# Performance work log

Hardware: AMD Instinct MI355X
Metric: run time of the kernel (lower is better)

## Reference

```python
import jax, jax.numpy as jnp
import numpy as np

D_MODEL = 2048
D_COMPARE = 2048
D_MEMORY = 2048
N_HEADS = 16
KV_HEADS = 4
KV_REPEAT = N_HEADS // KV_HEADS          # 4
C_HD = D_COMPARE // N_HEADS              # 128 compare head dim
M_HD = D_MEMORY // N_HEADS               # 128 memory head dim
TOTAL_OUT = D_COMPARE + KV_HEADS * C_HD + KV_HEADS * M_HD  # 3072


def setup_inputs() -> dict:
    key = jax.random.key(0)
    ks = jax.random.split(key, 5)
    b, t = 2, 2048
    x = jax.random.normal(ks[0], (b, t, D_MODEL), dtype=jnp.float32)
    s_in = 1.0 / np.sqrt(D_MODEL)
    s_out = 1.0 / np.sqrt(D_MEMORY)
    in_w = jax.random.uniform(ks[1], (TOTAL_OUT, D_MODEL), jnp.float32, -s_in, s_in)
    in_b = jax.random.uniform(ks[2], (TOTAL_OUT,), jnp.float32, -s_in, s_in)
    out_w = jax.random.uniform(ks[3], (D_MODEL, D_MEMORY), jnp.float32, -s_out, s_out)
    out_b = jax.random.uniform(ks[4], (D_MODEL,), jnp.float32, -s_out, s_out)
    return {"x": x, "in_w": in_w, "in_b": in_b, "out_w": out_w, "out_b": out_b}


def reference(x, in_w, in_b, out_w, out_b):
    b, t, _ = x.shape
    packed = jnp.einsum("btd,od->bto", x, in_w) + in_b          # [b,t,TOTAL_OUT]
    q, k, v = jnp.split(packed, [D_COMPARE, D_COMPARE + KV_HEADS * C_HD], axis=-1)
    # q: [b, kv, rep, t, hd] -- head h maps to kv group h // KV_REPEAT
    # (torch repeat_interleave on KV head dim == grouped reshape of q heads)
    q = q.reshape(b, t, KV_HEADS, KV_REPEAT, C_HD).transpose(0, 2, 3, 1, 4)
    k = k.reshape(b, t, KV_HEADS, C_HD).transpose(0, 2, 1, 3)   # [b,kv,t,hd]
    v = v.reshape(b, t, KV_HEADS, M_HD).transpose(0, 2, 1, 3)   # [b,kv,t,mhd]
    scale = 1.0 / np.sqrt(C_HD)
    scores = jnp.einsum("bgrqd,bgkd->bgrqk", q, k) * scale      # [b,kv,rep,t,t]
    attn = jax.nn.softmax(scores, axis=-1)
    y = jnp.einsum("bgrqk,bgkd->bgrqd", attn, v)                # [b,kv,rep,t,mhd]
    y = y.transpose(0, 3, 1, 2, 4).reshape(b, t, D_MEMORY)      # heads back in order
    return jnp.einsum("btm,dm->btd", y, out_w) + out_b
```

## Files before the change

kernel.cpp:

```cpp
#include <hip/hip_runtime.h>
#include <hip/hip_bf16.h>
#include <stdint.h>

#define DEV __device__ __forceinline__

typedef __attribute__((ext_vector_type(8))) short bf16x8;
typedef __attribute__((ext_vector_type(4))) float f32x4;
typedef __attribute__((ext_vector_type(16))) float f32x16;
typedef __attribute__((ext_vector_type(4))) unsigned u32x4;

DEV unsigned short f2bf(float f) {
  unsigned u = __builtin_bit_cast(unsigned, f);
  unsigned r = u + 0x7FFF + ((u >> 16) & 1);
  return (unsigned short)(r >> 16);
}

DEV unsigned short f2bfh(float f) {
  __bf16 h = (__bf16)f;
  return __builtin_bit_cast(unsigned short, h);
}

DEV unsigned cvtpk(float lo, float hi) {
  unsigned r;
  asm("v_cvt_pk_bf16_f32 %0, %1, %2" : "=v"(r) : "v"(lo), "v"(hi));
  return r;
}

DEV void plswap(unsigned &a, unsigned &b) {
  asm("v_permlane32_swap_b32 %0, %1" : "+v"(a), "+v"(b));
}

typedef __attribute__((address_space(1))) void gvoid;
typedef __attribute__((address_space(3))) void lvoid;

DEV void g2l16(const void* g, void* l) {
  __builtin_amdgcn_global_load_lds((gvoid*)g, (lvoid*)l, 16, 0, 0);
}

#define MFMA16(a, b, c) __builtin_amdgcn_mfma_f32_16x16x32_bf16(a, b, c, 0, 0, 0)
#define MFMA32(a, b, c) __builtin_amdgcn_mfma_f32_32x32x16_bf16(a, b, c, 0, 0, 0)

__global__ void k_cvt3(const float* __restrict__ x, unsigned short* __restrict__ xo, int nx4,
                       const float* __restrict__ w, unsigned short* __restrict__ wo, int nw4,
                       const float* __restrict__ v, unsigned short* __restrict__ vo, int nv4) {
  int i = blockIdx.x * blockDim.x + threadIdx.x;
  int stride = gridDim.x * blockDim.x;
  int tot = nx4 + nw4 + nv4;
  for (; i < tot; i += stride) {
    const float* src; unsigned short* dst; int j = i;
    if (j < nx4) { src = x; dst = xo; }
    else if ((j -= nx4) < nw4) { src = w; dst = wo; }
    else { j -= nw4; src = v; dst = vo; }
    float4 val = reinterpret_cast<const float4*>(src)[j];
    ushort4 o;
    o.x = f2bf(val.x); o.y = f2bf(val.y); o.z = f2bf(val.z); o.w = f2bf(val.w);
    reinterpret_cast<ushort4*>(dst)[j] = o;
  }
}

template<bool BF16OUT>
__global__ __launch_bounds__(256, 2) void k_gemm(
    const unsigned short* __restrict__ A, const unsigned short* __restrict__ B,
    const float* __restrict__ bias, void* __restrict__ C,
    int M, int N, int K) {
  __shared__ unsigned short As[128 * 32];
  __shared__ unsigned short Bs[128 * 32];
  int tid = threadIdx.x;
  int lane = tid & 63, wid = tid >> 6;
  int bm = blockIdx.y * 128, bn = blockIdx.x * 128;
  int wm = (wid >> 1) * 64, wn = (wid & 1) * 64;
  int row16 = lane & 15, kq = lane >> 4;
  f32x4 acc[4][4] = {};
  int r = tid >> 2, c = (tid & 3) * 8;
  const unsigned short* Ag = A + (size_t)(bm + r) * K + c;
  const unsigned short* Bg = B + (size_t)(bn + r) * K + c;
  for (int k0 = 0; k0 < K; k0 += 32) {
    g2l16(Ag + k0, &As[tid * 8]);
    g2l16(Ag + (size_t)64 * K + k0, &As[2048 + tid * 8]);
    g2l16(Bg + k0, &Bs[tid * 8]);
    g2l16(Bg + (size_t)64 * K + k0, &Bs[2048 + tid * 8]);
    __syncthreads();
    bf16x8 a[4], b[4];
#pragma unroll
    for (int m = 0; m < 4; m++) a[m] = *(const bf16x8*)&As[(wm + m * 16 + row16) * 32 + kq * 8];
#pragma unroll
    for (int n = 0; n < 4; n++) b[n] = *(const bf16x8*)&Bs[(wn + n * 16 + row16) * 32 + kq * 8];
    __builtin_amdgcn_s_setprio(1);
#pragma unroll
    for (int m = 0; m < 4; m++)
#pragma unroll
      for (int n = 0; n < 4; n++)
        acc[m][n] = MFMA16(a[m], b[n], acc[m][n]);
    __builtin_amdgcn_s_setprio(0);
    __syncthreads();
  }
#pragma unroll
  for (int n = 0; n < 4; n++) {
    int col = bn + wn + n * 16 + row16;
    float bv = bias[col];
#pragma unroll
    for (int m = 0; m < 4; m++) {
      int rw = bm + wm + m * 16 + kq * 4;
#pragma unroll
      for (int j = 0; j < 4; j++) {
        float v = acc[m][n][j] + bv;
        if (BF16OUT) ((unsigned short*)C)[(size_t)(rw + j) * N + col] = f2bf(v);
        else         ((float*)C)[(size_t)(rw + j) * N + col] = v;
      }
    }
  }
}

__global__ void k_pack(const unsigned short* __restrict__ packed, unsigned short* __restrict__ attp) {
  __shared__ unsigned short tile[64][136];
  int t = blockIdx.x, g = blockIdx.y;
  int b = g >> 2, kv = g & 3;
  int tid = threadIdx.x;
#pragma unroll
  for (int i = 0; i < 4; i++) {
    int tl = i * 16 + (tid >> 4);
    int d0 = (tid & 15) * 8;
    *(bf16x8*)&tile[tl][d0] =
        *(const bf16x8*)&packed[(size_t)(b * 2048 + t * 64 + tl) * 3072 + 2560 + kv * 128 + d0];
  }
  size_t obase = (size_t)(g * 32 + t) * 32 * 64 * 8;
#pragma unroll
  for (int f = 0; f < 4; f++) {
    int idx = f * 256 + tid;
    int frag = idx >> 6, lane = idx & 63;
    int l31 = lane & 31, h2 = lane >> 5;
    int kb2 = frag >> 3, kc = frag & 7;
    const unsigned short* src = &packed[(size_t)(b * 2048 + t * 64 + kb2 * 32 + l31) * 3072
                                        + 2048 + kv * 128 + (2 * kc + h2) * 8];
    *(bf16x8*)&attp[obase + (size_t)(frag * 64 + lane) * 8] = *(const bf16x8*)src;
  }
  __syncthreads();
#pragma unroll
  for (int f = 0; f < 4; f++) {
    int idx = f * 256 + tid;
    int f16 = idx >> 6, lane = idx & 63;
    int l31 = lane & 31, h2 = lane >> 5;
    int db = f16 >> 2, ks = f16 & 3;
    int d = 32 * db + l31;
    bf16x8 ov;
#pragma unroll
    for (int e = 0; e < 8; e++) ov[e] = (short)tile[(2 * ks + h2) * 8 + e][d];
    *(bf16x8*)&attp[obase + (size_t)((16 + f16) * 64 + lane) * 8] = ov;
  }
}

__global__ __launch_bounds__(256, 2) void k_flash(
    const unsigned short* __restrict__ packed,
    const unsigned short* __restrict__ attp,
    unsigned short* __restrict__ Y) {
  __shared__ unsigned short Qs[128 * 128];
  int tid = threadIdx.x, lane = tid & 63, wid = tid >> 6;
  int l31 = lane & 31, hi = lane >> 5;
  int kx = l31 & 15;
  int g = blockIdx.x;
  int s8 = g & 7;
  int b = s8 >> 2, kv = s8 & 3;
  int w = g >> 3;
  int h = kv * 4 + (w & 3);
  int qt = w >> 2;
  size_t prow = (size_t)b * 2048;

  {
    int rr = tid >> 4;
    int cc = ((tid & 15) ^ rr) * 8;
    const unsigned short* qg = packed + (prow + qt * 128 + rr) * 3072 + h * 128 + cc;
#pragma unroll
    for (int i = 0; i < 8; i++)
      g2l16(qg + (size_t)i * 16 * 3072, &Qs[i * 2048 + tid * 8]);
  }
  asm volatile("s_waitcnt vmcnt(0)" ::: "memory");
  __builtin_amdgcn_s_barrier();
  bf16x8 q[8];
  int qrow = wid * 32 + l31;
#pragma unroll
  for (int kc = 0; kc < 8; kc++)
    q[kc] = *(const bf16x8*)&Qs[qrow * 128 + (((2 * kc + hi) ^ kx) * 8)];
  asm volatile("s_waitcnt lgkmcnt(0)" ::: "memory");
  __builtin_amdgcn_sched_barrier(0);
  __builtin_amdgcn_s_barrier();

  const bf16x8* pk = (const bf16x8*)attp + ((size_t)s8 << 16);

  bf16x8 b0[4], b1[4], b2[4], b3[4];
#pragma unroll
  for (int j = 0; j < 4; j++) {
    b0[j] = pk[((0 + j) << 6) | lane];
    b1[j] = pk[((4 + j) << 6) | lane];
    b2[j] = pk[((8 + j) << 6) | lane];
    b3[j] = pk[((12 + j) << 6) | lane];
  }

  f32x16 o[4] = {};
  f32x16 ls = {};
  const float sc2 = 0.08838834764831845f * 1.4426950408889634f;
  const float MOFF = 14.f;
  bf16x8 ones;
#pragma unroll
  for (int e = 0; e < 8; e++) ones[e] = (short)0x3F80;

  for (int t = 0; t < 32; t++) {
    const bf16x8* pt  = pk + ((size_t)t << 11);
    const bf16x8* ptn = pk + ((size_t)(t < 31 ? t + 1 : 31) << 11);

    f32x16 st0 = {}, st1 = {};
    __builtin_amdgcn_s_setprio(1);
#pragma unroll
    for (int j = 0; j < 4; j++) st0 = MFMA32(b0[j], q[j], st0);
    __builtin_amdgcn_s_setprio(0);
#pragma unroll
    for (int j = 0; j < 4; j++) b0[j] = pt[((16 + j) << 6) | lane];
    __builtin_amdgcn_s_setprio(1);
#pragma unroll
    for (int j = 0; j < 4; j++) st0 = MFMA32(b1[j], q[4 + j], st0);
    __builtin_amdgcn_s_setprio(0);
#pragma unroll
    for (int j = 0; j < 4; j++) b1[j] = pt[((20 + j) << 6) | lane];
    __builtin_amdgcn_s_setprio(1);
#pragma unroll
    for (int j = 0; j < 4; j++) st1 = MFMA32(b2[j], q[j], st1);
    __builtin_amdgcn_s_setprio(0);
#pragma unroll
    for (int j = 0; j < 4; j++) b2[j] = pt[((24 + j) << 6) | lane];
    __builtin_amdgcn_s_setprio(1);
#pragma unroll
    for (int j = 0; j < 4; j++) st1 = MFMA32(b3[j], q[4 + j], st1);
    __builtin_amdgcn_s_setprio(0);
#pragma unroll
    for (int j = 0; j < 4; j++) b3[j] = pt[((28 + j) << 6) | lane];

#pragma unroll
    for (int r = 0; r < 16; r++) st0[r] = exp2f(fmaf(st0[r], sc2, -MOFF));
#pragma unroll
    for (int r = 0; r < 16; r++) st1[r] = exp2f(fmaf(st1[r], sc2, -MOFF));

    bf16x8 pf[4];
    {
      unsigned E0 = cvtpk(st0[0],  st0[1]);
      unsigned E1 = cvtpk(st0[2],  st0[3]);
      unsigned E2 = cvtpk(st0[4],  st0[5]);
      unsigned E3 = cvtpk(st0[6],  st0[7]);
      unsigned E4 = cvtpk(st0[8],  st0[9]);
      unsigned E5 = cvtpk(st0[10], st0[11]);
      unsigned E6 = cvtpk(st0[12], st0[13]);
      unsigned E7 = cvtpk(st0[14], st0[15]);
      plswap(E0, E2); plswap(E1, E3);
      plswap(E4, E6); plswap(E5, E7);
      pf[0] = __builtin_bit_cast(bf16x8, u32x4{E0, E1, E2, E3});
      pf[1] = __builtin_bit_cast(bf16x8, u32x4{E4, E5, E6, E7});
      unsigned F0 = cvtpk(st1[0],  st1[1]);
      unsigned F1 = cvtpk(st1[2],  st1[3]);
      unsigned F2 = cvtpk(st1[4],  st1[5]);
      unsigned F3 = cvtpk(st1[6],  st1[7]);
      unsigned F4 = cvtpk(st1[8],  st1[9]);
      unsigned F5 = cvtpk(st1[10], st1[11]);
      unsigned F6 = cvtpk(st1[12], st1[13]);
      unsigned F7 = cvtpk(st1[14], st1[15]);
      plswap(F0, F2); plswap(F1, F3);
      plswap(F4, F6); plswap(F5, F7);
      pf[2] = __builtin_bit_cast(bf16x8, u32x4{F0, F1, F2, F3});
      pf[3] = __builtin_bit_cast(bf16x8, u32x4{F4, F5, F6, F7});
    }

#pragma unroll
    for (int ks = 0; ks < 4; ks++) ls = MFMA32(pf[ks], ones, ls);

    __builtin_amdgcn_s_setprio(1);
#pragma unroll
    for (int j = 0; j < 4; j++) o[0] = MFMA32(pf[j], b0[j], o[0]);
    __builtin_amdgcn_s_setprio(0);
#pragma unroll
    for (int j = 0; j < 4; j++) b0[j] = ptn[((0 + j) << 6) | lane];
    __builtin_amdgcn_s_setprio(1);
#pragma unroll
    for (int j = 0; j < 4; j++) o[1] = MFMA32(pf[j], b1[j], o[1]);
    __builtin_amdgcn_s_setprio(0);
#pragma unroll
    for (int j = 0; j < 4; j++) b1[j] = ptn[((4 + j) << 6) | lane];
    __builtin_amdgcn_s_setprio(1);
#pragma unroll
    for (int j = 0; j < 4; j++) o[2] = MFMA32(pf[j], b2[j], o[2]);
    __builtin_amdgcn_s_setprio(0);
#pragma unroll
    for (int j = 0; j < 4; j++) b2[j] = ptn[((8 + j) << 6) | lane];
    __builtin_amdgcn_s_setprio(1);
#pragma unroll
    for (int j = 0; j < 4; j++) o[3] = MFMA32(pf[j], b3[j], o[3]);
    __builtin_amdgcn_s_setprio(0);
#pragma unroll
    for (int j = 0; j < 4; j++) b3[j] = ptn[((12 + j) << 6) | lane];

    __builtin_amdgcn_s_barrier();
  }

#pragma unroll
  for (int r = 0; r < 16; r++) {
    int ql = (r & 3) + 8 * (r >> 2) + 4 * hi;
    float inv = 1.f / ls[r];
    size_t orow = prow + (size_t)qt * 128 + wid * 32 + ql;
#pragma unroll
    for (int db = 0; db < 4; db++)
      Y[orow * 2048 + h * 128 + db * 32 + l31] = f2bfh(o[db][r] * inv);
  }
}

extern "C" void kernel_launch(void* const* d_in, const int* in_sizes, int n_in,
                              void* d_out, int out_size, void* d_ws, size_t ws_size,
                              hipStream_t stream) {
  const float* x     = (const float*)d_in[0];
  const float* in_w  = (const float*)d_in[1];
  const float* in_b  = (const float*)d_in[2];
  const float* out_w = (const float*)d_in[3];
  const float* out_b = (const float*)d_in[4];
  float* out = (float*)d_out;

  unsigned short* xb     = (unsigned short*)d_ws;
  unsigned short* wb     = xb + 8388608;
  unsigned short* owb    = wb + 6291456;
  unsigned short* packed = owb + 4194304;
  unsigned short* y      = packed + 12582912;
  unsigned short* attp   = xb;

  k_cvt3<<<dim3(2048), dim3(256), 0, stream>>>(x, xb, 8388608 / 4,
                                               in_w, wb, 6291456 / 4,
                                               out_w, owb, 4194304 / 4);

  k_gemm<true><<<dim3(24, 32), dim3(256), 0, stream>>>(xb, wb, in_b, packed, 4096, 3072, 2048);
  k_pack<<<dim3(32, 8), dim3(256), 0, stream>>>(packed, attp);
  k_flash<<<dim3(512), dim3(256), 0, stream>>>(packed, attp, y);
  k_gemm<false><<<dim3(16, 32), dim3(256), 0, stream>>>(y, owb, out_b, out, 4096, 2048, 2048);
}
```

Measured before the change: 222.3 us.

## Stage K tiles through double-buffered LDS and compute row sums with VALU

The flash kernel now loads K tiles from the packed attention buffer into a double-buffered LDS area with async global-to-LDS copies, two tiles ahead, and reads them from LDS. Previously every wave loaded K directly from global memory into registers. V still streams through registers one tile ahead, and S is split into two accumulators per half so the MFMA chains are shorter. The softmax row sum is now accumulated with VALU adds plus a cross-half shuffle, replacing the ones-vector MFMA, and is passed through LDS for the final normalisation. This cuts redundant global and L2 traffic for K shared across waves, but adds a barrier per iteration and LDS read traffic.

```diff
diff --git a/kernel.cpp b/kernel.cpp
--- a/kernel.cpp
+++ b/kernel.cpp
@@ -153,7 +153,7 @@
     const unsigned short* __restrict__ packed,
     const unsigned short* __restrict__ attp,
     unsigned short* __restrict__ Y) {
-  __shared__ unsigned short Qs[128 * 128];
+  __shared__ unsigned short Ks[2][8192];
   int tid = threadIdx.x, lane = tid & 63, wid = tid >> 6;
   int l31 = lane & 31, hi = lane >> 5;
   int kx = l31 & 15;
@@ -165,13 +165,14 @@
   int qt = w >> 2;
   size_t prow = (size_t)b * 2048;
 
+  unsigned short* Qsm = &Ks[0][0];
   {
     int rr = tid >> 4;
     int cc = ((tid & 15) ^ rr) * 8;
     const unsigned short* qg = packed + (prow + qt * 128 + rr) * 3072 + h * 128 + cc;
 #pragma unroll
     for (int i = 0; i < 8; i++)
-      g2l16(qg + (size_t)i * 16 * 3072, &Qs[i * 2048 + tid * 8]);
+      g2l16(qg + (size_t)i * 16 * 3072, &Qsm[i * 2048 + tid * 8]);
   }
   asm volatile("s_waitcnt vmcnt(0)" ::: "memory");
   __builtin_amdgcn_s_barrier();
@@ -179,64 +180,89 @@
   int qrow = wid * 32 + l31;
 #pragma unroll
   for (int kc = 0; kc < 8; kc++)
-    q[kc] = *(const bf16x8*)&Qs[qrow * 128 + (((2 * kc + hi) ^ kx) * 8)];
+    q[kc] = *(const bf16x8*)&Qsm[qrow * 128 + (((2 * kc + hi) ^ kx) * 8)];
   asm volatile("s_waitcnt lgkmcnt(0)" ::: "memory");
   __builtin_amdgcn_sched_barrier(0);
   __builtin_amdgcn_s_barrier();
 
-  const bf16x8* pk = (const bf16x8*)attp + ((size_t)s8 << 16);
-
-  bf16x8 b0[4], b1[4], b2[4], b3[4];
-#pragma unroll
-  for (int j = 0; j < 4; j++) {
-    b0[j] = pk[((0 + j) << 6) | lane];
-    b1[j] = pk[((4 + j) << 6) | lane];
-    b2[j] = pk[((8 + j) << 6) | lane];
-    b3[j] = pk[((12 + j) << 6) | lane];
-  }
+  const unsigned short* kst = attp + (size_t)s8 * 32 * 16384;
+  const bf16x8* vst = (const bf16x8*)attp;
+
+  auto stageK = [&](int t, int buf) {
+    const unsigned short* src = kst + (size_t)t * 16384 + tid * 8;
+#pragma unroll
+    for (int i = 0; i < 4; i++)
+      g2l16(src + i * 2048, &Ks[buf][i * 2048 + tid * 8]);
+  };
+
+  stageK(0, 0);
+  stageK(1, 1);
+  bf16x8 bv0[4], bv1[4], bv2[4], bv3[4];
+  {
+    size_t vb = (size_t)s8 * 32 * 2048 + 1024;
+#pragma unroll
+    for (int ks = 0; ks < 4; ks++) {
+      bv0[ks] = vst[vb + (0 * 4 + ks) * 64 + lane];
+      bv1[ks] = vst[vb + (1 * 4 + ks) * 64 + lane];
+      bv2[ks] = vst[vb + (2 * 4 + ks) * 64 + lane];
+      bv3[ks] = vst[vb + (3 * 4 + ks) * 64 + lane];
+    }
+  }
+  asm volatile("s_waitcnt vmcnt(20)" ::: "memory");
+  __builtin_amdgcn_s_barrier();
 
   f32x16 o[4] = {};
-  f32x16 ls = {};
+  float lr = 0.f;
   const float sc2 = 0.08838834764831845f * 1.4426950408889634f;
   const float MOFF = 14.f;
-  bf16x8 ones;
-#pragma unroll
-  for (int e = 0; e < 8; e++) ones[e] = (short)0x3F80;
 
   for (int t = 0; t < 32; t++) {
-    const bf16x8* pt  = pk + ((size_t)t << 11);
-    const bf16x8* ptn = pk + ((size_t)(t < 31 ? t + 1 : 31) << 11);
-
-    f32x16 st0 = {}, st1 = {};
-    __builtin_amdgcn_s_setprio(1);
-#pragma unroll
-    for (int j = 0; j < 4; j++) st0 = MFMA32(b0[j], q[j], st0);
-    __builtin_amdgcn_s_setprio(0);
-#pragma unroll
-    for (int j = 0; j < 4; j++) b0[j] = pt[((16 + j) << 6) | lane];
-    __builtin_amdgcn_s_setprio(1);
-#pragma unroll
-    for (int j = 0; j < 4; j++) st0 = MFMA32(b1[j], q[4 + j], st0);
-    __builtin_amdgcn_s_setprio(0);
-#pragma unroll
-    for (int j = 0; j < 4; j++) b1[j] = pt[((20 + j) << 6) | lane];
-    __builtin_amdgcn_s_setprio(1);
-#pragma unroll
-    for (int j = 0; j < 4; j++) st1 = MFMA32(b2[j], q[j], st1);
-    __builtin_amdgcn_s_setprio(0);
-#pragma unroll
-    for (int j = 0; j < 4; j++) b2[j] = pt[((24 + j) << 6) | lane];
-    __builtin_amdgcn_s_setprio(1);
-#pragma unroll
-    for (int j = 0; j < 4; j++) st1 = MFMA32(b3[j], q[4 + j], st1);
-    __builtin_amdgcn_s_setprio(0);
-#pragma unroll
-    for (int j = 0; j < 4; j++) b3[j] = pt[((28 + j) << 6) | lane];
-
-#pragma unroll
-    for (int r = 0; r < 16; r++) st0[r] = exp2f(fmaf(st0[r], sc2, -MOFF));
-#pragma unroll
-    for (int r = 0; r < 16; r++) st1[r] = exp2f(fmaf(st1[r], sc2, -MOFF));
+    int buf = t & 1;
+    int tn  = t < 31 ? t + 1 : 31;
+    int tn2 = t < 30 ? t + 2 : 31;
+
+    f32x16 sa0 = {}, sb0 = {}, sa1 = {}, sb1 = {};
+    {
+      bf16x8 ak[4];
+#pragma unroll
+      for (int kc = 0; kc < 4; kc++) ak[kc] = *(const bf16x8*)&Ks[buf][(kc * 64 + lane) * 8];
+      __builtin_amdgcn_s_setprio(1);
+#pragma unroll
+      for (int kc = 0; kc < 4; kc++) sa0 = MFMA32(ak[kc], q[kc], sa0);
+      __builtin_amdgcn_s_setprio(0);
+#pragma unroll
+      for (int kc = 0; kc < 4; kc++) ak[kc] = *(const bf16x8*)&Ks[buf][((4 + kc) * 64 + lane) * 8];
+      __builtin_amdgcn_s_setprio(1);
+#pragma unroll
+      for (int kc = 0; kc < 4; kc++) sb0 = MFMA32(ak[kc], q[4 + kc], sb0);
+      __builtin_amdgcn_s_setprio(0);
+#pragma unroll
+      for (int kc = 0; kc < 4; kc++) ak[kc] = *(const bf16x8*)&Ks[buf][((8 + kc) * 64 + lane) * 8];
+      __builtin_amdgcn_s_setprio(1);
+#pragma unroll
+      for (int kc = 0; kc < 4; kc++) sa1 = MFMA32(ak[kc], q[kc], sa1);
+      __builtin_amdgcn_s_setprio(0);
+#pragma unroll
+      for (int kc = 0; kc < 4; kc++) ak[kc] = *(const bf16x8*)&Ks[buf][((12 + kc) * 64 + lane) * 8];
+      __builtin_amdgcn_s_setprio(1);
+#pragma unroll
+      for (int kc = 0; kc < 4; kc++) sb1 = MFMA32(ak[kc], q[4 + kc], sb1);
+      __builtin_amdgcn_s_setprio(0);
+    }
+    __builtin_amdgcn_s_barrier();
+    stageK(tn2, buf);
+
+    f32x16 st0, st1;
+    float rs = 0.f;
+#pragma unroll
+    for (int r = 0; r < 16; r++) {
+      st0[r] = exp2f(fmaf(sa0[r] + sb0[r], sc2, -MOFF));
+      st1[r] = exp2f(fmaf(sa1[r] + sb1[r], sc2, -MOFF));
+    }
+#pragma unroll
+    for (int r = 0; r < 16; r++) rs += st0[r] + st1[r];
+    rs += __shfl_xor(rs, 32);
+    lr += rs;
 
     bf16x8 pf[4];
     {
@@ -266,41 +292,42 @@
       pf[3] = __builtin_bit_cast(bf16x8, u32x4{F4, F5, F6, F7});
     }
 
-#pragma unroll
-    for (int ks = 0; ks < 4; ks++) ls = MFMA32(pf[ks], ones, ls);
-
-    __builtin_amdgcn_s_setprio(1);
-#pragma unroll
-    for (int j = 0; j < 4; j++) o[0] = MFMA32(pf[j], b0[j], o[0]);
-    __builtin_amdgcn_s_setprio(0);
-#pragma unroll
-    for (int j = 0; j < 4; j++) b0[j] = ptn[((0 + j) << 6) | lane];
-    __builtin_amdgcn_s_setprio(1);
-#pragma unroll
-    for (int j = 0; j < 4; j++) o[1] = MFMA32(pf[j], b1[j], o[1]);
-    __builtin_amdgcn_s_setprio(0);
-#pragma unroll
-    for (int j = 0; j < 4; j++) b1[j] = ptn[((4 + j) << 6) | lane];
-    __builtin_amdgcn_s_setprio(1);
-#pragma unroll
-    for (int j = 0; j < 4; j++) o[2] = MFMA32(pf[j], b2[j], o[2]);
-    __builtin_amdgcn_s_setprio(0);
-#pragma unroll
-    for (int j = 0; j < 4; j++) b2[j] = ptn[((8 + j) << 6) | lane];
-    __builtin_amdgcn_s_setprio(1);
-#pragma unroll
-    for (int j = 0; j < 4; j++) o[3] = MFMA32(pf[j], b3[j], o[3]);
-    __builtin_amdgcn_s_setprio(0);
-#pragma unroll
-    for (int j = 0; j < 4; j++) b3[j] = ptn[((12 + j) << 6) | lane];
-
-    __builtin_amdgcn_s_barrier();
-  }
-
+    size_t vb = (size_t)(s8 * 32 + tn) * 2048 + 1024;
+    __builtin_amdgcn_s_setprio(1);
+#pragma unroll
+    for (int ks = 0; ks < 4; ks++) o[0] = MFMA32(pf[ks], bv0[ks], o[0]);
+    __builtin_amdgcn_s_setprio(0);
+#pragma unroll
+    for (int ks = 0; ks < 4; ks++) bv0[ks] = vst[vb + (0 * 4 + ks) * 64 + lane];
+    __builtin_amdgcn_s_setprio(1);
+#pragma unroll
+    for (int ks = 0; ks < 4; ks++) o[1] = MFMA32(pf[ks], bv1[ks], o[1]);
+    __builtin_amdgcn_s_setprio(0);
+#pragma unroll
+    for (int ks = 0; ks < 4; ks++) bv1[ks] = vst[vb + (1 * 4 + ks) * 64 + lane];
+    __builtin_amdgcn_s_setprio(1);
+#pragma unroll
+    for (int ks = 0; ks < 4; ks++) o[2] = MFMA32(pf[ks], bv2[ks], o[2]);
+    __builtin_amdgcn_s_setprio(0);
+#pragma unroll
+    for (int ks = 0; ks < 4; ks++) bv2[ks] = vst[vb + (2 * 4 + ks) * 64 + lane];
+    __builtin_amdgcn_s_setprio(1);
+#pragma unroll
+    for (int ks = 0; ks < 4; ks++) o[3] = MFMA32(pf[ks], bv3[ks], o[3]);
+    __builtin_amdgcn_s_setprio(0);
+#pragma unroll
+    for (int ks = 0; ks < 4; ks++) bv3[ks] = vst[vb + (3 * 4 + ks) * 64 + lane];
+
+    asm volatile("s_waitcnt vmcnt(20)" ::: "memory");
+  }
+  asm volatile("s_waitcnt vmcnt(0)" ::: "memory");
+
+  float* axc = (float*)&Ks[0][0] + wid * 32;
+  axc[l31] = lr;
 #pragma unroll
   for (int r = 0; r < 16; r++) {
     int ql = (r & 3) + 8 * (r >> 2) + 4 * hi;
-    float inv = 1.f / ls[r];
+    float inv = 1.f / axc[ql];
     size_t orow = prow + (size_t)qt * 128 + wid * 32 + ql;
 #pragma unroll
     for (int db = 0; db < 4; db++)
```

Measured after the change: 223.5 us. About the same (+0.5%).

## Replace GEMM with 8-wave triple-buffered 256x128 tiled kernel with XCD-aware block mapping

Applied to the files above, without the earlier changes.

Both projection GEMMs now use a 512-thread kernel with 256x128 output tiles, a 64-wide K step and a three-stage LDS ring buffer. Global-to-LDS prefetch is interleaved with MFMA phases under explicit barriers and waitcnts. LDS reads use XOR swizzling to avoid bank conflicts, and block IDs are remapped across the 8 XCDs to improve L2 reuse. The aim is to overlap memory latency with compute and raise arithmetic intensity, at the cost of higher LDS use (about 144KB per block) and more complex synchronisation.

```diff
diff --git a/kernel.cpp b/kernel.cpp
--- a/kernel.cpp
+++ b/kernel.cpp
@@ -59,47 +59,122 @@
 }
 
 template<bool BF16OUT>
-__global__ __launch_bounds__(256, 2) void k_gemm(
+__global__ __launch_bounds__(512, 2) void k_gemm8(
     const unsigned short* __restrict__ A, const unsigned short* __restrict__ B,
     const float* __restrict__ bias, void* __restrict__ C,
-    int M, int N, int K) {
-  __shared__ unsigned short As[128 * 32];
-  __shared__ unsigned short Bs[128 * 32];
-  int tid = threadIdx.x;
-  int lane = tid & 63, wid = tid >> 6;
-  int bm = blockIdx.y * 128, bn = blockIdx.x * 128;
-  int wm = (wid >> 1) * 64, wn = (wid & 1) * 64;
+    int M, int N, int K, int nbm) {
+  __shared__ unsigned short LA[3][16384];
+  __shared__ unsigned short LB[3][8192];
+  int tid = threadIdx.x, lane = tid & 63, wid = tid >> 6;
   int row16 = lane & 15, kq = lane >> 4;
-  f32x4 acc[4][4] = {};
-  int r = tid >> 2, c = (tid & 3) * 8;
-  const unsigned short* Ag = A + (size_t)(bm + r) * K + c;
-  const unsigned short* Bg = B + (size_t)(bn + r) * K + c;
-  for (int k0 = 0; k0 < K; k0 += 32) {
-    g2l16(Ag + k0, &As[tid * 8]);
-    g2l16(Ag + (size_t)64 * K + k0, &As[2048 + tid * 8]);
-    g2l16(Bg + k0, &Bs[tid * 8]);
-    g2l16(Bg + (size_t)64 * K + k0, &Bs[2048 + tid * 8]);
-    __syncthreads();
-    bf16x8 a[4], b[4];
-#pragma unroll
-    for (int m = 0; m < 4; m++) a[m] = *(const bf16x8*)&As[(wm + m * 16 + row16) * 32 + kq * 8];
-#pragma unroll
-    for (int n = 0; n < 4; n++) b[n] = *(const bf16x8*)&Bs[(wn + n * 16 + row16) * 32 + kq * 8];
-    __builtin_amdgcn_s_setprio(1);
+  int s7 = row16 & 7;
+  int qq = gridDim.x >> 3;
+  int wgid = (blockIdx.x & 7) * qq + (blockIdx.x >> 3);
+  int bm = (wgid % nbm) * 256;
+  int bn = (wgid / nbm) * 128;
+  int wm = (wid >> 2) * 128, wn = (wid & 3) * 32;
+
+  int srow = tid >> 3;
+  int schunk = ((tid & 7) ^ (srow & 7)) * 8;
+  const unsigned short* Asrc = A + (size_t)(bm + srow) * K + schunk;
+  const unsigned short* Bsrc = B + (size_t)(bn + srow) * K + schunk;
+  int ldst = tid * 8;
+
+  auto stgA = [&](int kt, int buf, int i) {
+    g2l16(Asrc + (size_t)i * 64 * K + kt * 64, &LA[buf][i * 4096 + ldst]);
+  };
+  auto stgB = [&](int kt, int buf, int i) {
+    g2l16(Bsrc + (size_t)i * 64 * K + kt * 64, &LB[buf][i * 4096 + ldst]);
+  };
+
+#pragma unroll
+  for (int i = 0; i < 4; i++) stgA(0, 0, i);
+  stgB(0, 0, 0); stgB(0, 0, 1);
+#pragma unroll
+  for (int i = 0; i < 4; i++) stgA(1, 1, i);
+  stgB(1, 1, 0); stgB(1, 1, 1);
+  asm volatile("s_waitcnt vmcnt(6)" ::: "memory");
+  __builtin_amdgcn_s_barrier();
+
+  f32x4 acc[8][2] = {};
+  int KS = K >> 6;
+  for (int kt = 0; kt < KS; ++kt) {
+    int rb = kt % 3;
+    int sb = (kt + 2) % 3;
+    int ks = (kt + 2 < KS) ? kt + 2 : KS - 1;
+
+    bf16x8 a[4][2], bb[2][2];
 #pragma unroll
     for (int m = 0; m < 4; m++)
 #pragma unroll
-      for (int n = 0; n < 4; n++)
-        acc[m][n] = MFMA16(a[m], b[n], acc[m][n]);
-    __builtin_amdgcn_s_setprio(0);
-    __syncthreads();
-  }
-#pragma unroll
-  for (int n = 0; n < 4; n++) {
+      for (int kk = 0; kk < 2; kk++)
+        a[m][kk] = *(const bf16x8*)&LA[rb][(wm + m * 16 + row16) * 64 + (((kk * 4 + kq) ^ s7) * 8)];
+#pragma unroll
+    for (int n = 0; n < 2; n++)
+#pragma unroll
+      for (int kk = 0; kk < 2; kk++)
+        bb[n][kk] = *(const bf16x8*)&LB[rb][(wn + n * 16 + row16) * 64 + (((kk * 4 + kq) ^ s7) * 8)];
+    stgA(ks, sb, 0); stgA(ks, sb, 1);
+    __builtin_amdgcn_s_barrier();
+    asm volatile("s_waitcnt lgkmcnt(0)" ::: "memory");
+    __builtin_amdgcn_sched_barrier(0);
+    __builtin_amdgcn_s_setprio(1);
+#pragma unroll
+    for (int m = 0; m < 4; m++) {
+      acc[m][0] = MFMA16(a[m][0], bb[0][0], acc[m][0]);
+      acc[m][0] = MFMA16(a[m][1], bb[0][1], acc[m][0]);
+    }
+    __builtin_amdgcn_s_setprio(0);
+    __builtin_amdgcn_s_barrier();
+
+    stgA(ks, sb, 2); stgA(ks, sb, 3);
+    __builtin_amdgcn_s_barrier();
+    __builtin_amdgcn_s_setprio(1);
+#pragma unroll
+    for (int m = 0; m < 4; m++) {
+      acc[m][1] = MFMA16(a[m][0], bb[1][0], acc[m][1]);
+      acc[m][1] = MFMA16(a[m][1], bb[1][1], acc[m][1]);
+    }
+    __builtin_amdgcn_s_setprio(0);
+    __builtin_amdgcn_s_barrier();
+
+#pragma unroll
+    for (int m = 0; m < 4; m++)
+#pragma unroll
+      for (int kk = 0; kk < 2; kk++)
+        a[m][kk] = *(const bf16x8*)&LA[rb][(wm + (m + 4) * 16 + row16) * 64 + (((kk * 4 + kq) ^ s7) * 8)];
+    stgB(ks, sb, 0);
+    __builtin_amdgcn_s_barrier();
+    asm volatile("s_waitcnt lgkmcnt(0)" ::: "memory");
+    __builtin_amdgcn_sched_barrier(0);
+    __builtin_amdgcn_s_setprio(1);
+#pragma unroll
+    for (int m = 0; m < 4; m++) {
+      acc[m + 4][0] = MFMA16(a[m][0], bb[0][0], acc[m + 4][0]);
+      acc[m + 4][0] = MFMA16(a[m][1], bb[0][1], acc[m + 4][0]);
+    }
+    __builtin_amdgcn_s_setprio(0);
+    __builtin_amdgcn_s_barrier();
+
+    stgB(ks, sb, 1);
+    __builtin_amdgcn_s_barrier();
+    __builtin_amdgcn_s_setprio(1);
+#pragma unroll
+    for (int m = 0; m < 4; m++) {
+      acc[m + 4][1] = MFMA16(a[m][0], bb[1][0], acc[m + 4][1]);
+      acc[m + 4][1] = MFMA16(a[m][1], bb[1][1], acc[m + 4][1]);
+    }
+    __builtin_amdgcn_s_setprio(0);
+    asm volatile("s_waitcnt vmcnt(6)" ::: "memory");
+    __builtin_amdgcn_s_barrier();
+  }
+
+#pragma unroll
+  for (int n = 0; n < 2; n++) {
     int col = bn + wn + n * 16 + row16;
     float bv = bias[col];
 #pragma unroll
-    for (int m = 0; m < 4; m++) {
+    for (int m = 0; m < 8; m++) {
       int rw = bm + wm + m * 16 + kq * 4;
 #pragma unroll
       for (int j = 0; j < 4; j++) {
@@ -159,8 +234,9 @@
   int kx = l31 & 15;
   int g = blockIdx.x;
   int s8 = g & 7;
-  int b = s8 >> 2, kv = s8 & 3;
+  int b = s8 >> 2;
   int w = g >> 3;
+  int kv = s8 & 3;
   int h = kv * 4 + (w & 3);
   int qt = w >> 2;
   size_t prow = (size_t)b * 2048;
@@ -329,8 +405,8 @@
                                                in_w, wb, 6291456 / 4,
                                                out_w, owb, 4194304 / 4);
 
-  k_gemm<true><<<dim3(24, 32), dim3(256), 0, stream>>>(xb, wb, in_b, packed, 4096, 3072, 2048);
+  k_gemm8<true><<<dim3(384), dim3(512), 0, stream>>>(xb, wb, in_b, packed, 4096, 3072, 2048, 16);
   k_pack<<<dim3(32, 8), dim3(256), 0, stream>>>(packed, attp);
   k_flash<<<dim3(512), dim3(256), 0, stream>>>(packed, attp, y);
-  k_gemm<false><<<dim3(16, 32), dim3(256), 0, stream>>>(y, owb, out_b, out, 4096, 2048, 2048);
-}
+  k_gemm8<false><<<dim3(256), dim3(512), 0, stream>>>(y, owb, out_b, out, 4096, 2048, 2048, 16);
+}
```

After: 250.4 us. +12.6%, slower.

## Stage K/V tiles in triple-buffered LDS shared by eight waves per block

Applied to the files above, without the earlier changes.

The flash kernel now runs 512-thread blocks covering 256 query rows, and the grid is halved to 256 blocks. Each K/V tile is copied once into LDS through triple-buffered global-to-LDS loads, and all eight waves read it from there instead of each wave streaming it from global memory into registers. QK for the next tile is issued before the softmax and PV of the current tile, giving a software pipeline. The aim is to cut global and L2 traffic and hide load latency, at the cost of 96KB of LDS per block, extra LDS reads and a vmcnt wait plus barrier every iteration.

```diff
diff --git a/kernel.cpp b/kernel.cpp
--- a/kernel.cpp
+++ b/kernel.cpp
@@ -149,11 +149,11 @@
   }
 }
 
-__global__ __launch_bounds__(256, 2) void k_flash(
+__global__ __launch_bounds__(512, 2) void k_flash8(
     const unsigned short* __restrict__ packed,
     const unsigned short* __restrict__ attp,
     unsigned short* __restrict__ Y) {
-  __shared__ unsigned short Qs[128 * 128];
+  __shared__ unsigned short S[49152];
   int tid = threadIdx.x, lane = tid & 63, wid = tid >> 6;
   int l31 = lane & 31, hi = lane >> 5;
   int kx = l31 & 15;
@@ -167,11 +167,11 @@
 
   {
     int rr = tid >> 4;
-    int cc = ((tid & 15) ^ rr) * 8;
-    const unsigned short* qg = packed + (prow + qt * 128 + rr) * 3072 + h * 128 + cc;
+    int cc = ((tid & 15) ^ (rr & 15)) * 8;
+    const unsigned short* qg = packed + (prow + qt * 256 + rr) * 3072 + h * 128 + cc;
 #pragma unroll
     for (int i = 0; i < 8; i++)
-      g2l16(qg + (size_t)i * 16 * 3072, &Qs[i * 2048 + tid * 8]);
+      g2l16(qg + (size_t)i * 32 * 3072, &S[i * 4096 + tid * 8]);
   }
   asm volatile("s_waitcnt vmcnt(0)" ::: "memory");
   __builtin_amdgcn_s_barrier();
@@ -179,21 +179,57 @@
   int qrow = wid * 32 + l31;
 #pragma unroll
   for (int kc = 0; kc < 8; kc++)
-    q[kc] = *(const bf16x8*)&Qs[qrow * 128 + (((2 * kc + hi) ^ kx) * 8)];
+    q[kc] = *(const bf16x8*)&S[qrow * 128 + (((2 * kc + hi) ^ kx) * 8)];
   asm volatile("s_waitcnt lgkmcnt(0)" ::: "memory");
   __builtin_amdgcn_sched_barrier(0);
   __builtin_amdgcn_s_barrier();
 
-  const bf16x8* pk = (const bf16x8*)attp + ((size_t)s8 << 16);
-
-  bf16x8 b0[4], b1[4], b2[4], b3[4];
-#pragma unroll
-  for (int j = 0; j < 4; j++) {
-    b0[j] = pk[((0 + j) << 6) | lane];
-    b1[j] = pk[((4 + j) << 6) | lane];
-    b2[j] = pk[((8 + j) << 6) | lane];
-    b3[j] = pk[((12 + j) << 6) | lane];
-  }
+  const unsigned short* tstr = attp + (size_t)s8 * 32 * 16384;
+
+  auto stage = [&](int t, int buf) {
+    const unsigned short* src = tstr + (size_t)t * 16384 + tid * 8;
+    unsigned short* dst = &S[buf * 16384 + tid * 8];
+#pragma unroll
+    for (int i = 0; i < 4; i++)
+      g2l16(src + i * 4096, dst + i * 4096);
+  };
+
+  auto qk = [&](int buf, f32x16& s0, f32x16& s1) {
+    const unsigned short* B = &S[buf * 16384];
+    bf16x8 ak[4];
+#pragma unroll
+    for (int j = 0; j < 4; j++) ak[j] = *(const bf16x8*)&B[((0 + j) * 64 + lane) * 8];
+    __builtin_amdgcn_s_setprio(1);
+#pragma unroll
+    for (int j = 0; j < 4; j++) s0 = MFMA32(ak[j], q[j], s0);
+    __builtin_amdgcn_s_setprio(0);
+#pragma unroll
+    for (int j = 0; j < 4; j++) ak[j] = *(const bf16x8*)&B[((4 + j) * 64 + lane) * 8];
+    __builtin_amdgcn_s_setprio(1);
+#pragma unroll
+    for (int j = 0; j < 4; j++) s0 = MFMA32(ak[j], q[4 + j], s0);
+    __builtin_amdgcn_s_setprio(0);
+#pragma unroll
+    for (int j = 0; j < 4; j++) ak[j] = *(const bf16x8*)&B[((8 + j) * 64 + lane) * 8];
+    __builtin_amdgcn_s_setprio(1);
+#pragma unroll
+    for (int j = 0; j < 4; j++) s1 = MFMA32(ak[j], q[j], s1);
+    __builtin_amdgcn_s_setprio(0);
+#pragma unroll
+    for (int j = 0; j < 4; j++) ak[j] = *(const bf16x8*)&B[((12 + j) * 64 + lane) * 8];
+    __builtin_amdgcn_s_setprio(1);
+#pragma unroll
+    for (int j = 0; j < 4; j++) s1 = MFMA32(ak[j], q[4 + j], s1);
+    __builtin_amdgcn_s_setprio(0);
+  };
+
+  stage(0, 0);
+  stage(1, 1);
+  asm volatile("s_waitcnt vmcnt(0)" ::: "memory");
+  __builtin_amdgcn_s_barrier();
+
+  f32x16 stc0 = {}, stc1 = {};
+  qk(0, stc0, stc1);
 
   f32x16 o[4] = {};
   f32x16 ls = {};
@@ -204,62 +240,40 @@
   for (int e = 0; e < 8; e++) ones[e] = (short)0x3F80;
 
   for (int t = 0; t < 32; t++) {
-    const bf16x8* pt  = pk + ((size_t)t << 11);
-    const bf16x8* ptn = pk + ((size_t)(t < 31 ? t + 1 : 31) << 11);
-
-    f32x16 st0 = {}, st1 = {};
-    __builtin_amdgcn_s_setprio(1);
-#pragma unroll
-    for (int j = 0; j < 4; j++) st0 = MFMA32(b0[j], q[j], st0);
-    __builtin_amdgcn_s_setprio(0);
-#pragma unroll
-    for (int j = 0; j < 4; j++) b0[j] = pt[((16 + j) << 6) | lane];
-    __builtin_amdgcn_s_setprio(1);
-#pragma unroll
-    for (int j = 0; j < 4; j++) st0 = MFMA32(b1[j], q[4 + j], st0);
-    __builtin_amdgcn_s_setprio(0);
-#pragma unroll
-    for (int j = 0; j < 4; j++) b1[j] = pt[((20 + j) << 6) | lane];
-    __builtin_amdgcn_s_setprio(1);
-#pragma unroll
-    for (int j = 0; j < 4; j++) st1 = MFMA32(b2[j], q[j], st1);
-    __builtin_amdgcn_s_setprio(0);
-#pragma unroll
-    for (int j = 0; j < 4; j++) b2[j] = pt[((24 + j) << 6) | lane];
-    __builtin_amdgcn_s_setprio(1);
-#pragma unroll
-    for (int j = 0; j < 4; j++) st1 = MFMA32(b3[j], q[4 + j], st1);
-    __builtin_amdgcn_s_setprio(0);
-#pragma unroll
-    for (int j = 0; j < 4; j++) b3[j] = pt[((28 + j) << 6) | lane];
-
-#pragma unroll
-    for (int r = 0; r < 16; r++) st0[r] = exp2f(fmaf(st0[r], sc2, -MOFF));
-#pragma unroll
-    for (int r = 0; r < 16; r++) st1[r] = exp2f(fmaf(st1[r], sc2, -MOFF));
+    int tn2 = t + 2 <= 31 ? t + 2 : 31;
+
+    stage(tn2, (t + 2) % 3);
+
+    f32x16 sn0 = {}, sn1 = {};
+    qk((t + 1) % 3, sn0, sn1);
+
+#pragma unroll
+    for (int r = 0; r < 16; r++) stc0[r] = exp2f(fmaf(stc0[r], sc2, -MOFF));
+#pragma unroll
+    for (int r = 0; r < 16; r++) stc1[r] = exp2f(fmaf(stc1[r], sc2, -MOFF));
 
     bf16x8 pf[4];
     {
-      unsigned E0 = cvtpk(st0[0],  st0[1]);
-      unsigned E1 = cvtpk(st0[2],  st0[3]);
-      unsigned E2 = cvtpk(st0[4],  st0[5]);
-      unsigned E3 = cvtpk(st0[6],  st0[7]);
-      unsigned E4 = cvtpk(st0[8],  st0[9]);
-      unsigned E5 = cvtpk(st0[10], st0[11]);
-      unsigned E6 = cvtpk(st0[12], st0[13]);
-      unsigned E7 = cvtpk(st0[14], st0[15]);
+      unsigned E0 = cvtpk(stc0[0],  stc0[1]);
+      unsigned E1 = cvtpk(stc0[2],  stc0[3]);
+      unsigned E2 = cvtpk(stc0[4],  stc0[5]);
+      unsigned E3 = cvtpk(stc0[6],  stc0[7]);
+      unsigned E4 = cvtpk(stc0[8],  stc0[9]);
+      unsigned E5 = cvtpk(stc0[10], stc0[11]);
+      unsigned E6 = cvtpk(stc0[12], stc0[13]);
+      unsigned E7 = cvtpk(stc0[14], stc0[15]);
       plswap(E0, E2); plswap(E1, E3);
       plswap(E4, E6); plswap(E5, E7);
       pf[0] = __builtin_bit_cast(bf16x8, u32x4{E0, E1, E2, E3});
       pf[1] = __builtin_bit_cast(bf16x8, u32x4{E4, E5, E6, E7});
-      unsigned F0 = cvtpk(st1[0],  st1[1]);
-      unsigned F1 = cvtpk(st1[2],  st1[3]);
-      unsigned F2 = cvtpk(st1[4],  st1[5]);
-      unsigned F3 = cvtpk(st1[6],  st1[7]);
-      unsigned F4 = cvtpk(st1[8],  st1[9]);
-      unsigned F5 = cvtpk(st1[10], st1[11]);
-      unsigned F6 = cvtpk(st1[12], st1[13]);
-      unsigned F7 = cvtpk(st1[14], st1[15]);
+      unsigned F0 = cvtpk(stc1[0],  stc1[1]);
+      unsigned F1 = cvtpk(stc1[2],  stc1[3]);
+      unsigned F2 = cvtpk(stc1[4],  stc1[5]);
+      unsigned F3 = cvtpk(stc1[6],  stc1[7]);
+      unsigned F4 = cvtpk(stc1[8],  stc1[9]);
+      unsigned F5 = cvtpk(stc1[10], stc1[11]);
+      unsigned F6 = cvtpk(stc1[12], stc1[13]);
+      unsigned F7 = cvtpk(stc1[14], stc1[15]);
       plswap(F0, F2); plswap(F1, F3);
       plswap(F4, F6); plswap(F5, F7);
       pf[2] = __builtin_bit_cast(bf16x8, u32x4{F0, F1, F2, F3});
@@ -268,32 +282,25 @@
 
 #pragma unroll
     for (int ks = 0; ks < 4; ks++) ls = MFMA32(pf[ks], ones, ls);
-
-    __builtin_amdgcn_s_setprio(1);
-#pragma unroll
-    for (int j = 0; j < 4; j++) o[0] = MFMA32(pf[j], b0[j], o[0]);
-    __builtin_amdgcn_s_setprio(0);
-#pragma unroll
-    for (int j = 0; j < 4; j++) b0[j] = ptn[((0 + j) << 6) | lane];
-    __builtin_amdgcn_s_setprio(1);
-#pragma unroll
-    for (int j = 0; j < 4; j++) o[1] = MFMA32(pf[j], b1[j], o[1]);
-    __builtin_amdgcn_s_setprio(0);
-#pragma unroll
-    for (int j = 0; j < 4; j++) b1[j] = ptn[((4 + j) << 6) | lane];
-    __builtin_amdgcn_s_setprio(1);
-#pragma unroll
-    for (int j = 0; j < 4; j++) o[2] = MFMA32(pf[j], b2[j], o[2]);
-    __builtin_amdgcn_s_setprio(0);
-#pragma unroll
-    for (int j = 0; j < 4; j++) b2[j] = ptn[((8 + j) << 6) | lane];
-    __builtin_amdgcn_s_setprio(1);
-#pragma unroll
-    for (int j = 0; j < 4; j++) o[3] = MFMA32(pf[j], b3[j], o[3]);
-    __builtin_amdgcn_s_setprio(0);
-#pragma unroll
-    for (int j = 0; j < 4; j++) b3[j] = ptn[((12 + j) << 6) | lane];
-
+    {
+      const unsigned short* B = &S[(t % 3) * 16384];
+#pragma unroll
+      for (int db = 0; db < 4; db++) {
+        bf16x8 bv[4];
+#pragma unroll
+        for (int ks = 0; ks < 4; ks++)
+          bv[ks] = *(const bf16x8*)&B[((16 + db * 4 + ks) * 64 + lane) * 8];
+        __builtin_amdgcn_s_setprio(1);
+#pragma unroll
+        for (int ks = 0; ks < 4; ks++) o[db] = MFMA32(pf[ks], bv[ks], o[db]);
+        __builtin_amdgcn_s_setprio(0);
+      }
+    }
+
+    stc0 = sn0;
+    stc1 = sn1;
+
+    asm volatile("s_waitcnt vmcnt(0)" ::: "memory");
     __builtin_amdgcn_s_barrier();
   }
 
@@ -301,7 +308,7 @@
   for (int r = 0; r < 16; r++) {
     int ql = (r & 3) + 8 * (r >> 2) + 4 * hi;
     float inv = 1.f / ls[r];
-    size_t orow = prow + (size_t)qt * 128 + wid * 32 + ql;
+    size_t orow = prow + (size_t)qt * 256 + wid * 32 + ql;
 #pragma unroll
     for (int db = 0; db < 4; db++)
       Y[orow * 2048 + h * 128 + db * 32 + l31] = f2bfh(o[db][r] * inv);
@@ -331,6 +338,6 @@
 
   k_gemm<true><<<dim3(24, 32), dim3(256), 0, stream>>>(xb, wb, in_b, packed, 4096, 3072, 2048);
   k_pack<<<dim3(32, 8), dim3(256), 0, stream>>>(packed, attp);
-  k_flash<<<dim3(512), dim3(256), 0, stream>>>(packed, attp, y);
+  k_flash8<<<dim3(256), dim3(512), 0, stream>>>(packed, attp, y);
   k_gemm<false><<<dim3(16, 32), dim3(256), 0, stream>>>(y, owb, out_b, out, 4096, 2048, 2048);
 }
```

New measurement: 218.1 us. About the same (-1.9%).
